# Kernel optimization log

Hardware: AMD Instinct MI355X
Metric: run time of the kernel (lower is better)

## Reference

```python
import jax, jax.numpy as jnp
import numpy as np
import math

B, S, E, H = 2, 2048, 1024, 16
D = E // H  # head_dim = 64


def setup_inputs() -> dict:
    key = jax.random.key(0)
    ks = jax.random.split(key, 5)
    scale_p = 1.0 / math.sqrt(D)
    return {
        "x": jax.random.normal(ks[0], (B, S, E), dtype=jnp.float32),
        "Wq": jax.random.normal(ks[1], (D, D), dtype=jnp.float32) * scale_p,
        "Wk": jax.random.normal(ks[2], (D, D), dtype=jnp.float32) * scale_p,
        "Wv": jax.random.normal(ks[3], (D, D), dtype=jnp.float32) * scale_p,
        "W_out": jax.random.normal(ks[4], (E, E), dtype=jnp.float32) * (1.0 / math.sqrt(E)),
        "b_out": jnp.zeros((E,), dtype=jnp.float32),
    }


def reference(x, Wq, Wk, Wv, W_out, b_out):
    b, s, e = x.shape
    xh = x.reshape(b, s, H, D)  # [B,S,H,D]
    # per-head linear projections (torch Linear: y = x @ W.T), weights shared across heads
    q = jnp.einsum("bshd,ed->bshe", xh, Wq)
    k = jnp.einsum("bshd,ed->bshe", xh, Wk)
    v = jnp.einsum("bshd,ed->bshe", xh, Wv)
    # scaled dot-product attention, scale = sqrt(embed_dim) per tutorial-style impl
    energy = jnp.einsum("bqhd,bkhd->bhqk", q, k) / jnp.sqrt(jnp.float32(e))
    attn = jax.nn.softmax(energy, axis=-1)  # [B,H,S,S]
    out = jnp.einsum("bhqk,bkhd->bqhd", attn, v).reshape(b, s, e)
    return out @ W_out.T + b_out
```

## Files before the change

kernel.cpp:

```cpp
#include <hip/hip_runtime.h>
#include <math.h>

#define BB 2
#define SS 2048
#define EE 1024
#define HH 16
#define DD 64
constexpr int NROWS = BB * SS * HH;
constexpr float SCALE_Q = 1.4426950408889634f / 32.0f;

typedef __attribute__((ext_vector_type(8))) short bf16x8;
typedef __attribute__((ext_vector_type(4))) float f32x4;
typedef __attribute__((ext_vector_type(16))) float f32x16;
typedef __attribute__((ext_vector_type(4))) unsigned u32x4;

__device__ inline ushort f2bf(float f) {
  unsigned u = __builtin_bit_cast(unsigned, f);
  u += 0x7fffu + ((u >> 16) & 1u);
  return (ushort)(u >> 16);
}

__device__ inline unsigned cvt_pk(float lo, float hi) {
  unsigned r;
  asm("v_cvt_pk_bf16_f32 %0, %1, %2" : "=v"(r) : "v"(lo), "v"(hi));
  return r;
}

__global__ __launch_bounds__(256) void wconv(
    const float* __restrict__ Wq, const float* __restrict__ Wk,
    const float* __restrict__ Wv, const float* __restrict__ Wo,
    ushort* __restrict__ wqkvb, ushort* __restrict__ wob) {
  int idx = blockIdx.x * 256 + threadIdx.x;
  const float* sp;
  ushort* dp;
  if (idx < 1536) {
    int t = idx >> 9, j = idx & 511;
    const float* W = (t == 0) ? Wq : ((t == 1) ? Wk : Wv);
    sp = W + j * 8;
    dp = wqkvb + t * 4096 + j * 8;
  } else {
    size_t j = (size_t)(idx - 1536) * 8;
    sp = Wo + j;
    dp = wob + j;
  }
  float4 a = *(const float4*)sp;
  float4 c = *(const float4*)(sp + 4);
  u32x4 r;
  r[0] = cvt_pk(a.x, a.y);
  r[1] = cvt_pk(a.z, a.w);
  r[2] = cvt_pk(c.x, c.y);
  r[3] = cvt_pk(c.z, c.w);
  *(u32x4*)dp = r;
}

__global__ __launch_bounds__(256) void qkv_mfma(
    const float* __restrict__ x, const ushort* __restrict__ wqkv,
    ushort* __restrict__ qo, ushort* __restrict__ ko, ushort* __restrict__ vto) {
  __shared__ __align__(16) ushort Xs[128 * 72];
  __shared__ __align__(16) ushort Ws[3][64 * 72];
  const int tid = threadIdx.x, w = tid >> 6, l = tid & 63;
  const int g = l >> 4, c = l & 15;
  const int s0 = blockIdx.x * 128, h = blockIdx.y, b = blockIdx.z;

  for (int i = tid; i < 1536; i += 256) {
    int t = i >> 9, j = i & 511;
    int r = j >> 3, e0 = (j & 7) * 8;
    *(bf16x8*)&Ws[t][r * 72 + e0] = *(const bf16x8*)&wqkv[t * 4096 + r * 64 + e0];
  }
  for (int i = tid; i < 2048; i += 256) {
    int r = i >> 4, c4 = (i & 15) * 4;
    float4 xv = *(const float4*)&x[(((size_t)b * SS + s0 + r) * HH + h) * DD + c4];
    uint2 pk;
    pk.x = cvt_pk(xv.x, xv.y);
    pk.y = cvt_pk(xv.z, xv.w);
    *(uint2*)&Xs[r * 72 + c4] = pk;
  }
  __syncthreads();

  bf16x8 a_[2][2];
#pragma unroll
  for (int rf = 0; rf < 2; ++rf) {
    a_[rf][0] = *(bf16x8*)&Xs[(w * 32 + rf * 16 + c) * 72 + g * 8];
    a_[rf][1] = *(bf16x8*)&Xs[(w * 32 + rf * 16 + c) * 72 + 32 + g * 8];
  }

#pragma unroll
  for (int t = 0; t < 2; ++t) {
    ushort* out = (t == 0) ? qo : ko;
    const float sc = (t == 0) ? SCALE_Q : 1.0f;
#pragma unroll
    for (int ct = 0; ct < 4; ++ct) {
      bf16x8 b0 = *(bf16x8*)&Ws[t][(ct * 16 + c) * 72 + g * 8];
      bf16x8 b1 = *(bf16x8*)&Ws[t][(ct * 16 + c) * 72 + 32 + g * 8];
#pragma unroll
      for (int rf = 0; rf < 2; ++rf) {
        f32x4 acc = (f32x4){0.f, 0.f, 0.f, 0.f};
        acc = __builtin_amdgcn_mfma_f32_16x16x32_bf16(b0, a_[rf][0], acc, 0, 0, 0);
        acc = __builtin_amdgcn_mfma_f32_16x16x32_bf16(b1, a_[rf][1], acc, 0, 0, 0);
        uint2 pk;
        pk.x = cvt_pk(acc[0] * sc, acc[1] * sc);
        pk.y = cvt_pk(acc[2] * sc, acc[3] * sc);
        int srow = s0 + w * 32 + rf * 16 + c;
        *(uint2*)&out[((size_t)b * SS + srow) * EE + h * DD + ct * 16 + g * 4] = pk;
      }
    }
  }
#pragma unroll
  for (int ct = 0; ct < 4; ++ct) {
    bf16x8 b0 = *(bf16x8*)&Ws[2][(ct * 16 + c) * 72 + g * 8];
    bf16x8 b1 = *(bf16x8*)&Ws[2][(ct * 16 + c) * 72 + 32 + g * 8];
#pragma unroll
    for (int rf = 0; rf < 2; ++rf) {
      f32x4 acc = (f32x4){0.f, 0.f, 0.f, 0.f};
      acc = __builtin_amdgcn_mfma_f32_16x16x32_bf16(a_[rf][0], b0, acc, 0, 0, 0);
      acc = __builtin_amdgcn_mfma_f32_16x16x32_bf16(a_[rf][1], b1, acc, 0, 0, 0);
      uint2 pk;
      pk.x = cvt_pk(acc[0], acc[1]);
      pk.y = cvt_pk(acc[2], acc[3]);
      int d = ct * 16 + c;
      int srow = w * 32 + rf * 16 + g * 4;
      *(uint2*)&vto[(((size_t)b * HH + h) * DD + d) * SS + s0 + srow] = pk;
    }
  }
}

__global__ __launch_bounds__(256) void attn_mfma(
    const ushort* __restrict__ q, const ushort* __restrict__ k,
    const ushort* __restrict__ vt, ushort* __restrict__ o) {
  __shared__ __align__(16) ushort Ks[2][64 * 72];
  __shared__ __align__(16) ushort Vts[2][64 * 72];
  const int tid = threadIdx.x, w = tid >> 6, l = tid & 63;
  const int lq = l & 31, h2 = l >> 5;
  const int work = ((blockIdx.x & 7) << 6) | (blockIdx.x >> 3);
  const int qt = work & 15, hb = work >> 4;
  const int h = hb & 15, b = hb >> 4;
  const int q0 = qt * 128 + w * 32;

  const size_t bh_qk = (size_t)b * SS * EE + h * DD;
  const size_t bh_vt = (size_t)b * SS * EE + h * (DD * SS);

  const int sr0 = tid >> 3;
  const int se0 = (tid & 7) * 8;
  const int krow0 = (sr0 & 19) | ((sr0 & 4) << 1) | ((sr0 & 8) >> 1);

  {
    bf16x8 kr0 = *(const bf16x8*)&k[bh_qk + (size_t)sr0 * EE + se0];
    bf16x8 kr1 = *(const bf16x8*)&k[bh_qk + (size_t)(sr0 + 32) * EE + se0];
    bf16x8 vr0 = *(const bf16x8*)&vt[bh_vt + (size_t)sr0 * SS + se0];
    bf16x8 vr1 = *(const bf16x8*)&vt[bh_vt + (size_t)(sr0 + 32) * SS + se0];
    *(bf16x8*)&Ks[0][krow0 * 72 + se0] = kr0;
    *(bf16x8*)&Ks[0][(krow0 + 32) * 72 + se0] = kr1;
    *(bf16x8*)&Vts[0][sr0 * 72 + se0] = vr0;
    *(bf16x8*)&Vts[0][(sr0 + 32) * 72 + se0] = vr1;
  }

  bf16x8 aq[4];
#pragma unroll
  for (int db = 0; db < 4; ++db)
    aq[db] = *(const bf16x8*)&q[bh_qk + (size_t)(q0 + lq) * EE + db * 16 + h2 * 8];

  f32x16 accO[2];
  float lacc[2] = {0.f, 0.f};
#pragma unroll
  for (int ct = 0; ct < 2; ++ct)
#pragma unroll
    for (int r = 0; r < 16; ++r) accO[ct][r] = 0.f;

  u32x4 pwvP[2][2];
  bf16x8 vfP[2][4];

  __syncthreads();

  {
    bf16x8 kr0 = *(const bf16x8*)&k[bh_qk + (size_t)(64 + sr0) * EE + se0];
    bf16x8 kr1 = *(const bf16x8*)&k[bh_qk + (size_t)(64 + sr0 + 32) * EE + se0];
    bf16x8 vr0 = *(const bf16x8*)&vt[bh_vt + 64 + (size_t)sr0 * SS + se0];
    bf16x8 vr1 = *(const bf16x8*)&vt[bh_vt + 64 + (size_t)(sr0 + 32) * SS + se0];

    f32x16 s[2];
#pragma unroll
    for (int kb = 0; kb < 2; ++kb) {
      f32x16 acc;
#pragma unroll
      for (int r = 0; r < 16; ++r) acc[r] = 0.f;
#pragma unroll
      for (int db = 0; db < 4; ++db) {
        bf16x8 ka = *(bf16x8*)&Ks[0][(kb * 32 + lq) * 72 + db * 16 + h2 * 8];
        acc = __builtin_amdgcn_mfma_f32_32x32x16_bf16(ka, aq[db], acc, 0, 0, 0);
      }
      s[kb] = acc;
    }
#pragma unroll
    for (int kb = 0; kb < 2; ++kb)
#pragma unroll
      for (int t16 = 0; t16 < 2; ++t16)
#pragma unroll
        for (int j2 = 0; j2 < 4; ++j2) {
          float pa = __builtin_amdgcn_exp2f(s[kb][t16 * 8 + j2 * 2]);
          float pb = __builtin_amdgcn_exp2f(s[kb][t16 * 8 + j2 * 2 + 1]);
          lacc[kb] += pa + pb;
          pwvP[kb][t16][j2] = cvt_pk(pa, pb);
        }
#pragma unroll
    for (int ct = 0; ct < 2; ++ct)
#pragma unroll
      for (int kb = 0; kb < 2; ++kb)
#pragma unroll
        for (int t16 = 0; t16 < 2; ++t16)
          vfP[ct][kb * 2 + t16] = *(bf16x8*)&Vts[0][(ct * 32 + lq) * 72 +
                                                    kb * 32 + t16 * 16 + h2 * 8];
    *(bf16x8*)&Ks[1][krow0 * 72 + se0] = kr0;
    *(bf16x8*)&Ks[1][(krow0 + 32) * 72 + se0] = kr1;
    *(bf16x8*)&Vts[1][sr0 * 72 + se0] = vr0;
    *(bf16x8*)&Vts[1][(sr0 + 32) * 72 + se0] = vr1;
    __syncthreads();
  }

  for (int t = 1; t < 32; ++t) {
    const int cur = t & 1;
    const int tn = (t + 1) & 31;

    bf16x8 kr0, kr1, vr0, vr1;
    {
      const size_t kb2 = bh_qk + (size_t)(tn * 64) * EE;
      kr0 = *(const bf16x8*)&k[kb2 + (size_t)sr0 * EE + se0];
      kr1 = *(const bf16x8*)&k[kb2 + (size_t)(sr0 + 32) * EE + se0];
      const size_t vb2 = bh_vt + tn * 64;
      vr0 = *(const bf16x8*)&vt[vb2 + (size_t)sr0 * SS + se0];
      vr1 = *(const bf16x8*)&vt[vb2 + (size_t)(sr0 + 32) * SS + se0];
    }

#pragma unroll
    for (int ct = 0; ct < 2; ++ct)
#pragma unroll
      for (int kb = 0; kb < 2; ++kb)
#pragma unroll
        for (int t16 = 0; t16 < 2; ++t16)
          accO[ct] = __builtin_amdgcn_mfma_f32_32x32x16_bf16(
              vfP[ct][kb * 2 + t16],
              __builtin_bit_cast(bf16x8, pwvP[kb][t16]), accO[ct], 0, 0, 0);

    f32x16 s[2];
#pragma unroll
    for (int kb = 0; kb < 2; ++kb) {
      f32x16 acc;
#pragma unroll
      for (int r = 0; r < 16; ++r) acc[r] = 0.f;
#pragma unroll
      for (int db = 0; db < 4; ++db) {
        bf16x8 ka = *(bf16x8*)&Ks[cur][(kb * 32 + lq) * 72 + db * 16 + h2 * 8];
        acc = __builtin_amdgcn_mfma_f32_32x32x16_bf16(ka, aq[db], acc, 0, 0, 0);
      }
      s[kb] = acc;
    }

    u32x4 pwvC[2][2];
#pragma unroll
    for (int kb = 0; kb < 2; ++kb)
#pragma unroll
      for (int t16 = 0; t16 < 2; ++t16)
#pragma unroll
        for (int j2 = 0; j2 < 4; ++j2) {
          float pa = __builtin_amdgcn_exp2f(s[kb][t16 * 8 + j2 * 2]);
          float pb = __builtin_amdgcn_exp2f(s[kb][t16 * 8 + j2 * 2 + 1]);
          lacc[kb] += pa + pb;
          pwvC[kb][t16][j2] = cvt_pk(pa, pb);
        }

#pragma unroll
    for (int ct = 0; ct < 2; ++ct)
#pragma unroll
      for (int kb = 0; kb < 2; ++kb)
#pragma unroll
        for (int t16 = 0; t16 < 2; ++t16)
          vfP[ct][kb * 2 + t16] = *(bf16x8*)&Vts[cur][(ct * 32 + lq) * 72 +
                                                      kb * 32 + t16 * 16 + h2 * 8];

    {
      const int nxt = cur ^ 1;
      *(bf16x8*)&Ks[nxt][krow0 * 72 + se0] = kr0;
      *(bf16x8*)&Ks[nxt][(krow0 + 32) * 72 + se0] = kr1;
      *(bf16x8*)&Vts[nxt][sr0 * 72 + se0] = vr0;
      *(bf16x8*)&Vts[nxt][(sr0 + 32) * 72 + se0] = vr1;
    }
    __syncthreads();

#pragma unroll
    for (int kb = 0; kb < 2; ++kb)
#pragma unroll
      for (int t16 = 0; t16 < 2; ++t16) pwvP[kb][t16] = pwvC[kb][t16];
  }

#pragma unroll
  for (int ct = 0; ct < 2; ++ct)
#pragma unroll
    for (int kb = 0; kb < 2; ++kb)
#pragma unroll
      for (int t16 = 0; t16 < 2; ++t16)
        accO[ct] = __builtin_amdgcn_mfma_f32_32x32x16_bf16(
            vfP[ct][kb * 2 + t16],
            __builtin_bit_cast(bf16x8, pwvP[kb][t16]), accO[ct], 0, 0, 0);

  {
    float tsum = lacc[0] + lacc[1];
    tsum += __shfl_xor(tsum, 32, 64);
    float inv = 1.f / tsum;
    size_t row = (size_t)b * SS + q0 + lq;
#pragma unroll
    for (int ct = 0; ct < 2; ++ct)
#pragma unroll
      for (int rq = 0; rq < 4; ++rq) {
        uint2 pk;
        pk.x = cvt_pk(accO[ct][rq * 4 + 0] * inv, accO[ct][rq * 4 + 1] * inv);
        pk.y = cvt_pk(accO[ct][rq * 4 + 2] * inv, accO[ct][rq * 4 + 3] * inv);
        *(uint2*)&o[row * EE + h * DD + ct * 32 + rq * 8 + h2 * 4] = pk;
      }
  }
}

__global__ __launch_bounds__(256) void out_proj_mfma(
    const ushort* __restrict__ a, const ushort* __restrict__ wo,
    const float* __restrict__ bias, float* __restrict__ y) {
  __shared__ __align__(16) ushort As[2][128 * 72];
  __shared__ __align__(16) ushort Ws[2][64 * 72];
  const int tid = threadIdx.x, w = tid >> 6, l = tid & 63;
  const int g = l >> 4, c = l & 15;
  const int m0 = blockIdx.x * 128, n0 = blockIdx.y * 64;
  const int sr = tid >> 3, se = (tid & 7) * 8;

  f32x4 acc[2][4];
#pragma unroll
  for (int mf = 0; mf < 2; ++mf)
#pragma unroll
    for (int ct = 0; ct < 4; ++ct) acc[mf][ct] = (f32x4){0.f, 0.f, 0.f, 0.f};

  {
#pragma unroll
    for (int j = 0; j < 4; ++j) {
      int r = sr + j * 32;
      *(bf16x8*)&As[0][r * 72 + se] = *(const bf16x8*)&a[(size_t)(m0 + r) * EE + se];
    }
#pragma unroll
    for (int j = 0; j < 2; ++j) {
      int r = sr + j * 32;
      *(bf16x8*)&Ws[0][r * 72 + se] = *(const bf16x8*)&wo[(size_t)(n0 + r) * EE + se];
    }
  }
  __syncthreads();

  for (int t = 0; t < 16; ++t) {
    const int cur = t & 1;
    bf16x8 Arg[4], Brg[2];
    if (t < 15) {
      const int k0 = (t + 1) * 64;
#pragma unroll
      for (int j = 0; j < 4; ++j) {
        int r = sr + j * 32;
        Arg[j] = *(const bf16x8*)&a[(size_t)(m0 + r) * EE + k0 + se];
      }
#pragma unroll
      for (int j = 0; j < 2; ++j) {
        int r = sr + j * 32;
        Brg[j] = *(const bf16x8*)&wo[(size_t)(n0 + r) * EE + k0 + se];
      }
    }

    bf16x8 af[2][2];
#pragma unroll
    for (int mf = 0; mf < 2; ++mf) {
      af[mf][0] = *(bf16x8*)&As[cur][(w * 32 + mf * 16 + c) * 72 + g * 8];
      af[mf][1] = *(bf16x8*)&As[cur][(w * 32 + mf * 16 + c) * 72 + 32 + g * 8];
    }
    __builtin_amdgcn_s_setprio(1);
#pragma unroll
    for (int ct = 0; ct < 4; ++ct) {
      bf16x8 b0 = *(bf16x8*)&Ws[cur][(ct * 16 + c) * 72 + g * 8];
      bf16x8 b1 = *(bf16x8*)&Ws[cur][(ct * 16 + c) * 72 + 32 + g * 8];
#pragma unroll
      for (int mf = 0; mf < 2; ++mf) {
        acc[mf][ct] = __builtin_amdgcn_mfma_f32_16x16x32_bf16(af[mf][0], b0, acc[mf][ct], 0, 0, 0);
        acc[mf][ct] = __builtin_amdgcn_mfma_f32_16x16x32_bf16(af[mf][1], b1, acc[mf][ct], 0, 0, 0);
      }
    }
    __builtin_amdgcn_s_setprio(0);

    if (t < 15) {
      const int nxt = cur ^ 1;
#pragma unroll
      for (int j = 0; j < 4; ++j) {
        int r = sr + j * 32;
        *(bf16x8*)&As[nxt][r * 72 + se] = Arg[j];
      }
#pragma unroll
      for (int j = 0; j < 2; ++j) {
        int r = sr + j * 32;
        *(bf16x8*)&Ws[nxt][r * 72 + se] = Brg[j];
      }
    }
    __syncthreads();
  }

#pragma unroll
  for (int ct = 0; ct < 4; ++ct) {
    float bv = bias[n0 + ct * 16 + c];
#pragma unroll
    for (int mf = 0; mf < 2; ++mf)
#pragma unroll
      for (int r = 0; r < 4; ++r)
        y[(size_t)(m0 + w * 32 + mf * 16 + g * 4 + r) * EE + n0 + ct * 16 + c] =
            acc[mf][ct][r] + bv;
  }
}

extern "C" void kernel_launch(void* const* d_in, const int* in_sizes, int n_in,
                              void* d_out, int out_size, void* d_ws,
                              size_t ws_size, hipStream_t stream) {
  const float* x = (const float*)d_in[0];
  const float* Wq = (const float*)d_in[1];
  const float* Wk = (const float*)d_in[2];
  const float* Wv = (const float*)d_in[3];
  const float* Wo = (const float*)d_in[4];
  const float* bo = (const float*)d_in[5];
  float* out = (float*)d_out;

  const size_t per = (size_t)NROWS * 64;
  ushort* qb = (ushort*)d_ws;
  ushort* kb = qb + per;
  ushort* vtb = kb + per;
  ushort* aob = vtb + per;
  ushort* wob = aob + per;
  ushort* wqkvb = wob + 1024 * 1024;

  wconv<<<518, 256, 0, stream>>>(Wq, Wk, Wv, Wo, wqkvb, wob);
  qkv_mfma<<<dim3(16, 16, 2), 256, 0, stream>>>(x, wqkvb, qb, kb, vtb);
  attn_mfma<<<512, 256, 0, stream>>>(qb, kb, vtb, aob);
  out_proj_mfma<<<dim3(32, 16), 256, 0, stream>>>(aob, wob, bo, out);
}
```

Baseline: 81.29 us.

## Fuse weight conversion into QKV kernel and use 32x32 MFMA in out-projection

The separate weight-conversion kernel is removed. Each QKV block now converts its own slice of W_out to bf16 and converts Wq/Wk/Wv directly while loading them into shared memory, which saves one kernel launch and a global round trip. The output projection switches from 16x16x32 to 32x32x16 MFMA with weights as the A operand, permuting weight rows in LDS so the 32x32 accumulator layout gives contiguous columns per lane. This allows vectorized float4 stores of output and bias. The cost is that every QKV block redundantly converts the small per-head weights.

```diff
diff --git a/kernel.cpp b/kernel.cpp
--- a/kernel.cpp
+++ b/kernel.cpp
@@ -14,58 +14,49 @@
 typedef __attribute__((ext_vector_type(16))) float f32x16;
 typedef __attribute__((ext_vector_type(4))) unsigned u32x4;
 
-__device__ inline ushort f2bf(float f) {
-  unsigned u = __builtin_bit_cast(unsigned, f);
-  u += 0x7fffu + ((u >> 16) & 1u);
-  return (ushort)(u >> 16);
-}
-
 __device__ inline unsigned cvt_pk(float lo, float hi) {
   unsigned r;
   asm("v_cvt_pk_bf16_f32 %0, %1, %2" : "=v"(r) : "v"(lo), "v"(hi));
   return r;
 }
 
-__global__ __launch_bounds__(256) void wconv(
+__global__ __launch_bounds__(256) void qkv_mfma(
+    const float* __restrict__ x,
     const float* __restrict__ Wq, const float* __restrict__ Wk,
     const float* __restrict__ Wv, const float* __restrict__ Wo,
-    ushort* __restrict__ wqkvb, ushort* __restrict__ wob) {
-  int idx = blockIdx.x * 256 + threadIdx.x;
-  const float* sp;
-  ushort* dp;
-  if (idx < 1536) {
-    int t = idx >> 9, j = idx & 511;
-    const float* W = (t == 0) ? Wq : ((t == 1) ? Wk : Wv);
-    sp = W + j * 8;
-    dp = wqkvb + t * 4096 + j * 8;
-  } else {
-    size_t j = (size_t)(idx - 1536) * 8;
-    sp = Wo + j;
-    dp = wob + j;
-  }
-  float4 a = *(const float4*)sp;
-  float4 c = *(const float4*)(sp + 4);
-  u32x4 r;
-  r[0] = cvt_pk(a.x, a.y);
-  r[1] = cvt_pk(a.z, a.w);
-  r[2] = cvt_pk(c.x, c.y);
-  r[3] = cvt_pk(c.z, c.w);
-  *(u32x4*)dp = r;
-}
-
-__global__ __launch_bounds__(256) void qkv_mfma(
-    const float* __restrict__ x, const ushort* __restrict__ wqkv,
-    ushort* __restrict__ qo, ushort* __restrict__ ko, ushort* __restrict__ vto) {
+    ushort* __restrict__ qo, ushort* __restrict__ ko, ushort* __restrict__ vto,
+    ushort* __restrict__ wob) {
   __shared__ __align__(16) ushort Xs[128 * 72];
   __shared__ __align__(16) ushort Ws[3][64 * 72];
   const int tid = threadIdx.x, w = tid >> 6, l = tid & 63;
   const int g = l >> 4, c = l & 15;
   const int s0 = blockIdx.x * 128, h = blockIdx.y, b = blockIdx.z;
 
+  {
+    const int lin = blockIdx.x + (blockIdx.y << 4) + (blockIdx.z << 8);
+    const size_t base = (size_t)lin * 2048 + tid * 8;
+    float4 a = *(const float4*)&Wo[base];
+    float4 cc = *(const float4*)&Wo[base + 4];
+    u32x4 r;
+    r[0] = cvt_pk(a.x, a.y);
+    r[1] = cvt_pk(a.z, a.w);
+    r[2] = cvt_pk(cc.x, cc.y);
+    r[3] = cvt_pk(cc.z, cc.w);
+    *(u32x4*)&wob[base] = r;
+  }
+
   for (int i = tid; i < 1536; i += 256) {
     int t = i >> 9, j = i & 511;
     int r = j >> 3, e0 = (j & 7) * 8;
-    *(bf16x8*)&Ws[t][r * 72 + e0] = *(const bf16x8*)&wqkv[t * 4096 + r * 64 + e0];
+    const float* W = (t == 0) ? Wq : ((t == 1) ? Wk : Wv);
+    float4 va = *(const float4*)&W[r * 64 + e0];
+    float4 vb = *(const float4*)&W[r * 64 + e0 + 4];
+    u32x4 pk;
+    pk[0] = cvt_pk(va.x, va.y);
+    pk[1] = cvt_pk(va.z, va.w);
+    pk[2] = cvt_pk(vb.x, vb.y);
+    pk[3] = cvt_pk(vb.z, vb.w);
+    *(u32x4*)&Ws[t][r * 72 + e0] = pk;
   }
   for (int i = tid; i < 2048; i += 256) {
     int r = i >> 4, c4 = (i & 15) * 4;
@@ -324,15 +315,16 @@
   __shared__ __align__(16) ushort As[2][128 * 72];
   __shared__ __align__(16) ushort Ws[2][64 * 72];
   const int tid = threadIdx.x, w = tid >> 6, l = tid & 63;
-  const int g = l >> 4, c = l & 15;
+  const int lq = l & 31, h2 = l >> 5;
   const int m0 = blockIdx.x * 128, n0 = blockIdx.y * 64;
   const int sr = tid >> 3, se = (tid & 7) * 8;
-
-  f32x4 acc[2][4];
-#pragma unroll
-  for (int mf = 0; mf < 2; ++mf)
-#pragma unroll
-    for (int ct = 0; ct < 4; ++ct) acc[mf][ct] = (f32x4){0.f, 0.f, 0.f, 0.f};
+  const int krow = (sr & 19) | ((sr & 4) << 1) | ((sr & 8) >> 1);
+
+  f32x16 acc[2];
+#pragma unroll
+  for (int kb = 0; kb < 2; ++kb)
+#pragma unroll
+    for (int r = 0; r < 16; ++r) acc[kb][r] = 0.f;
 
   {
 #pragma unroll
@@ -340,11 +332,9 @@
       int r = sr + j * 32;
       *(bf16x8*)&As[0][r * 72 + se] = *(const bf16x8*)&a[(size_t)(m0 + r) * EE + se];
     }
-#pragma unroll
-    for (int j = 0; j < 2; ++j) {
-      int r = sr + j * 32;
-      *(bf16x8*)&Ws[0][r * 72 + se] = *(const bf16x8*)&wo[(size_t)(n0 + r) * EE + se];
-    }
+    *(bf16x8*)&Ws[0][krow * 72 + se] = *(const bf16x8*)&wo[(size_t)(n0 + sr) * EE + se];
+    *(bf16x8*)&Ws[0][(krow + 32) * 72 + se] =
+        *(const bf16x8*)&wo[(size_t)(n0 + sr + 32) * EE + se];
   }
   __syncthreads();
 
@@ -358,31 +348,21 @@
         int r = sr + j * 32;
         Arg[j] = *(const bf16x8*)&a[(size_t)(m0 + r) * EE + k0 + se];
       }
-#pragma unroll
-      for (int j = 0; j < 2; ++j) {
-        int r = sr + j * 32;
-        Brg[j] = *(const bf16x8*)&wo[(size_t)(n0 + r) * EE + k0 + se];
-      }
-    }
-
-    bf16x8 af[2][2];
-#pragma unroll
-    for (int mf = 0; mf < 2; ++mf) {
-      af[mf][0] = *(bf16x8*)&As[cur][(w * 32 + mf * 16 + c) * 72 + g * 8];
-      af[mf][1] = *(bf16x8*)&As[cur][(w * 32 + mf * 16 + c) * 72 + 32 + g * 8];
-    }
-    __builtin_amdgcn_s_setprio(1);
-#pragma unroll
-    for (int ct = 0; ct < 4; ++ct) {
-      bf16x8 b0 = *(bf16x8*)&Ws[cur][(ct * 16 + c) * 72 + g * 8];
-      bf16x8 b1 = *(bf16x8*)&Ws[cur][(ct * 16 + c) * 72 + 32 + g * 8];
-#pragma unroll
-      for (int mf = 0; mf < 2; ++mf) {
-        acc[mf][ct] = __builtin_amdgcn_mfma_f32_16x16x32_bf16(af[mf][0], b0, acc[mf][ct], 0, 0, 0);
-        acc[mf][ct] = __builtin_amdgcn_mfma_f32_16x16x32_bf16(af[mf][1], b1, acc[mf][ct], 0, 0, 0);
-      }
-    }
-    __builtin_amdgcn_s_setprio(0);
+      Brg[0] = *(const bf16x8*)&wo[(size_t)(n0 + sr) * EE + k0 + se];
+      Brg[1] = *(const bf16x8*)&wo[(size_t)(n0 + sr + 32) * EE + k0 + se];
+    }
+
+    bf16x8 af[4];
+#pragma unroll
+    for (int db = 0; db < 4; ++db)
+      af[db] = *(bf16x8*)&As[cur][(w * 32 + lq) * 72 + db * 16 + h2 * 8];
+#pragma unroll
+    for (int kb = 0; kb < 2; ++kb)
+#pragma unroll
+      for (int db = 0; db < 4; ++db) {
+        bf16x8 wf = *(bf16x8*)&Ws[cur][(kb * 32 + lq) * 72 + db * 16 + h2 * 8];
+        acc[kb] = __builtin_amdgcn_mfma_f32_32x32x16_bf16(wf, af[db], acc[kb], 0, 0, 0);
+      }
 
     if (t < 15) {
       const int nxt = cur ^ 1;
@@ -391,25 +371,27 @@
         int r = sr + j * 32;
         *(bf16x8*)&As[nxt][r * 72 + se] = Arg[j];
       }
-#pragma unroll
-      for (int j = 0; j < 2; ++j) {
-        int r = sr + j * 32;
-        *(bf16x8*)&Ws[nxt][r * 72 + se] = Brg[j];
-      }
+      *(bf16x8*)&Ws[nxt][krow * 72 + se] = Brg[0];
+      *(bf16x8*)&Ws[nxt][(krow + 32) * 72 + se] = Brg[1];
     }
     __syncthreads();
   }
 
-#pragma unroll
-  for (int ct = 0; ct < 4; ++ct) {
-    float bv = bias[n0 + ct * 16 + c];
-#pragma unroll
-    for (int mf = 0; mf < 2; ++mf)
-#pragma unroll
-      for (int r = 0; r < 4; ++r)
-        y[(size_t)(m0 + w * 32 + mf * 16 + g * 4 + r) * EE + n0 + ct * 16 + c] =
-            acc[mf][ct][r] + bv;
-  }
+  const size_t row = (size_t)(m0 + w * 32 + lq) * EE;
+#pragma unroll
+  for (int kb = 0; kb < 2; ++kb)
+#pragma unroll
+    for (int t16 = 0; t16 < 2; ++t16) {
+      const int nb = n0 + kb * 32 + t16 * 16 + h2 * 8;
+      float4 bv0 = *(const float4*)&bias[nb];
+      float4 bv1 = *(const float4*)&bias[nb + 4];
+      float4 o0 = {acc[kb][t16 * 8 + 0] + bv0.x, acc[kb][t16 * 8 + 1] + bv0.y,
+                   acc[kb][t16 * 8 + 2] + bv0.z, acc[kb][t16 * 8 + 3] + bv0.w};
+      float4 o1 = {acc[kb][t16 * 8 + 4] + bv1.x, acc[kb][t16 * 8 + 5] + bv1.y,
+                   acc[kb][t16 * 8 + 6] + bv1.z, acc[kb][t16 * 8 + 7] + bv1.w};
+      *(float4*)&y[row + nb] = o0;
+      *(float4*)&y[row + nb + 4] = o1;
+    }
 }
 
 extern "C" void kernel_launch(void* const* d_in, const int* in_sizes, int n_in,
@@ -429,10 +411,9 @@
   ushort* vtb = kb + per;
   ushort* aob = vtb + per;
   ushort* wob = aob + per;
-  ushort* wqkvb = wob + 1024 * 1024;
-
-  wconv<<<518, 256, 0, stream>>>(Wq, Wk, Wv, Wo, wqkvb, wob);
-  qkv_mfma<<<dim3(16, 16, 2), 256, 0, stream>>>(x, wqkvb, qb, kb, vtb);
+
+  qkv_mfma<<<dim3(16, 16, 2), 256, 0, stream>>>(x, Wq, Wk, Wv, Wo,
+                                                qb, kb, vtb, wob);
   attn_mfma<<<512, 256, 0, stream>>>(qb, kb, vtb, aob);
   out_proj_mfma<<<dim3(32, 16), 256, 0, stream>>>(aob, wob, bo, out);
 }
```

Result: faster. 78.53 us (-3.4%).
